# Kernel tuning notes

Hardware: AMD Instinct MI355X
Metric: run time of the kernel (lower is better)

The kernel has to match this reference:

```python
import jax, jax.numpy as jnp
import numpy as np

EPS = 1e-5

def setup_inputs() -> dict:
    key = jax.random.key(0)
    ks = jax.random.split(key, 12)
    b, C, Hx = 8, 1024, 28          # x: (b, C, Hx, Hx); y: (b, C//2, 2*Hx, 2*Hx)
    C2 = C // 2
    r = C2 // 7                      # fc bottleneck = 73
    f32 = jnp.float32
    inp = {
        'y': jax.random.normal(ks[0], (b, C2, 2*Hx, 2*Hx), f32),
        'x': jax.random.normal(ks[1], (b, C, Hx, Hx), f32),
        'fc1_w': jax.random.normal(ks[2], (r, C2), f32) * 0.02,
        'fc2_w': jax.random.normal(ks[3], (C2, r), f32) * 0.02,
        'conv_w': jax.random.normal(ks[4], (C2, C, 1, 1), f32) * 0.02,
        'conv_b': jnp.zeros((C2,), f32),
        'conv1_w': jax.random.normal(ks[5], (C2, C2 * 4, 1, 1), f32) * 0.02,
        'conv1_b': jnp.zeros((C2,), f32),
        'bn_gamma': jnp.ones((C2,), f32),
        'bn_beta': jnp.zeros((C2,), f32),
        'bn_mean': jnp.zeros((C2,), f32),
        'bn_var': jnp.ones((C2,), f32),
        'dw_w': jax.random.normal(ks[6], (C, 1, 3, 3), f32) * 0.1,  # depthwise, groups=C
        'dw_b': jnp.zeros((C,), f32),
    }
    return inp

def reference(y, x, fc1_w, fc2_w, conv_w, conv_b, conv1_w, conv1_b,
              bn_gamma, bn_beta, bn_mean, bn_var, dw_w, dw_b):
    def bn(t):  # BatchNorm2d in eval mode (running stats); same bn module reused twice
        return (t - bn_mean[:, None, None]) * jax.lax.rsqrt(bn_var[:, None, None] + EPS) \
               * bn_gamma[:, None, None] + bn_beta[:, None, None]
    # SE channel attention on y
    s = jnp.mean(y, axis=(2, 3))                              # (b, C2) GAP
    s = jax.nn.relu(s @ fc1_w.T) @ fc2_w.T                    # bias-free FCs
    y1 = y * jax.nn.sigmoid(s)[:, :, None, None]
    # depthwise 3x3 conv on x
    x1 = jax.lax.conv_general_dilated(
        x, dw_w, (1, 1), ((1, 1), (1, 1)),
        feature_group_count=x.shape[1],
        dimension_numbers=('NCHW', 'OIHW', 'NCHW')) + dw_b[None, :, None, None]
    # np.cov per (b, c) map: rows are variables, ddof=1 -> (Xc @ Xc^T)/(W-1)
    Wn = x1.shape[-1]
    xc = x1 - jnp.mean(x1, axis=-1, keepdims=True)
    x2 = jnp.einsum('bchw,bcgw->bchg', xc, xc) / (Wn - 1)     # (b, C, H, H)
    # 1x1 conv C->C2, bn, sigmoid
    x2 = jnp.einsum('bchw,oc->bohw', x2, conv_w[:, :, 0, 0]) + conv_b[None, :, None, None]
    x2 = jax.nn.sigmoid(bn(x2))
    # bilinear upsample x2 (half-pixel == torch align_corners=False)
    def up2(t):
        bb, cc, hh, ww = t.shape
        return jax.image.resize(t, (bb, cc, 2 * hh, 2 * ww), method='bilinear')
    x_up = up2(x)
    x2_up = up2(x2)
    cat = jnp.concatenate([y1, x2_up, x_up], axis=1)          # (b, 4*C2, 2H, 2W)
    out = jnp.einsum('bchw,oc->bohw', cat, conv1_w[:, :, 0, 0]) + conv1_b[None, :, None, None]
    return jax.nn.relu(bn(out))
```

## Files before the change

kernel.cpp:

```cpp
#include <hip/hip_runtime.h>
#include <math.h>

#define EPSV 1e-5f
#define B 8
#define C 1024
#define C2 512
#define RK 73
#define HW 784
#define QW 3136

typedef __attribute__((ext_vector_type(8))) short bf16x8;
typedef __attribute__((ext_vector_type(4))) float f32x4;

__device__ __forceinline__ unsigned short f2bf(float f) {
    unsigned u = __float_as_uint(f);
    return (unsigned short)((u + 0x7fffu + ((u >> 16) & 1u)) >> 16);
}
__device__ __forceinline__ float ld_f(const float* p) { return *p; }
__device__ __forceinline__ float ld_f(const unsigned short* p) {
    return __uint_as_float(((unsigned)*p) << 16);
}

__global__ void gap_kernel(const float* __restrict__ y, float* __restrict__ s0) {
    int bc = blockIdx.x;
    const float* p = y + (size_t)bc * QW;
    float sum = 0.f;
    for (int i = threadIdx.x; i < QW; i += 256) sum += p[i];
    for (int off = 32; off > 0; off >>= 1) sum += __shfl_down(sum, off, 64);
    __shared__ float red[4];
    if ((threadIdx.x & 63) == 0) red[threadIdx.x >> 6] = sum;
    __syncthreads();
    if (threadIdx.x == 0)
        s0[bc] = (red[0] + red[1] + red[2] + red[3]) * (1.0f / QW);
}

__global__ void se_fc_kernel(const float* __restrict__ s0,
                             const float* __restrict__ fc1_w,
                             const float* __restrict__ fc2_w,
                             float* __restrict__ att) {
    int b = blockIdx.x;
    __shared__ float sv[C2];
    __shared__ float hv[RK];
    for (int i = threadIdx.x; i < C2; i += 256) sv[i] = s0[b * C2 + i];
    __syncthreads();
    if (threadIdx.x < RK) {
        float acc = 0.f;
        const float* wr = fc1_w + threadIdx.x * C2;
        for (int k = 0; k < C2; ++k) acc += wr[k] * sv[k];
        hv[threadIdx.x] = fmaxf(acc, 0.f);
    }
    __syncthreads();
    for (int o = threadIdx.x; o < C2; o += 256) {
        float acc = 0.f;
        const float* wr = fc2_w + o * RK;
        for (int j = 0; j < RK; ++j) acc += wr[j] * hv[j];
        att[b * C2 + o] = 1.f / (1.f + expf(-acc));
    }
}

__global__ void dwcov_kernel(const float* __restrict__ x,
                             const float* __restrict__ dw_w,
                             const float* __restrict__ dw_b,
                             unsigned short* __restrict__ cov) {
    int bc = blockIdx.x;
    int c = bc & (C - 1);
    __shared__ float xs[HW];
    __shared__ float x1[HW];
    __shared__ float rm[28];
    const float* px = x + (size_t)bc * HW;
    for (int i = threadIdx.x; i < HW; i += 256) xs[i] = px[i];
    float wk[9];
#pragma unroll
    for (int j = 0; j < 9; ++j) wk[j] = dw_w[c * 9 + j];
    float bias = dw_b[c];
    __syncthreads();
    for (int p = threadIdx.x; p < HW; p += 256) {
        int h = p / 28, w = p - h * 28;
        float acc = bias;
#pragma unroll
        for (int dh = 0; dh < 3; ++dh) {
            int hh = h + dh - 1;
            if (hh < 0 || hh >= 28) continue;
#pragma unroll
            for (int dw = 0; dw < 3; ++dw) {
                int ww = w + dw - 1;
                if (ww < 0 || ww >= 28) continue;
                acc += xs[hh * 28 + ww] * wk[dh * 3 + dw];
            }
        }
        x1[p] = acc;
    }
    __syncthreads();
    if (threadIdx.x < 28) {
        float s = 0.f;
        for (int w = 0; w < 28; ++w) s += x1[threadIdx.x * 28 + w];
        rm[threadIdx.x] = s * (1.f / 28.f);
    }
    __syncthreads();
    unsigned short* pc = cov + (size_t)bc * HW;
    for (int p = threadIdx.x; p < HW; p += 256) {
        int h = p / 28, g = p - h * 28;
        float mh = rm[h], mg = rm[g];
        float acc = 0.f;
        for (int w = 0; w < 28; ++w)
            acc += (x1[h * 28 + w] - mh) * (x1[g * 28 + w] - mg);
        pc[p] = f2bf(acc * (1.f / 27.f));
    }
}

__global__ void pack_w(const float* __restrict__ conv_w, const float* __restrict__ conv_b,
                       const float* __restrict__ conv1_w, const float* __restrict__ conv1_b,
                       const float* __restrict__ bn_g, const float* __restrict__ bn_b,
                       const float* __restrict__ bn_m, const float* __restrict__ bn_v,
                       unsigned short* __restrict__ w0b, unsigned short* __restrict__ w1p0,
                       unsigned short* __restrict__ w1pT,
                       float* __restrict__ sA, float* __restrict__ sB0, float* __restrict__ sB1) {
    int o = blockIdx.x, t = threadIdx.x;
    for (int i = t; i < C; i += 256) w0b[(size_t)o * C + i] = f2bf(conv_w[(size_t)o * C + i]);
    for (int i = t; i < C2; i += 256) w1p0[(size_t)o * C2 + i] = f2bf(conv1_w[(size_t)o * 2048 + i]);
    for (int i = t; i < 1536; i += 256) w1pT[(size_t)o * 1536 + i] = f2bf(conv1_w[(size_t)o * 2048 + 512 + i]);
    if (t == 0) {
        float sc = rsqrtf(bn_v[o] + EPSV) * bn_g[o];
        float bi = bn_b[o] - bn_m[o] * sc;
        sA[o] = sc;
        sB0[o] = conv_b[o] * sc + bi;
        sB1[o] = conv1_b[o] * sc + bi;
    }
}

template<typename ST, bool ATT>
__global__ __launch_bounds__(256)
void transpose_pass(const ST* __restrict__ src, unsigned short* __restrict__ dst,
                    const float* __restrict__ att,
                    int rows, int cols, int dpitch, int doff) {
    int b = blockIdx.z;
    int c0 = blockIdx.y * 64, p0 = blockIdx.x * 64;
    __shared__ float ts[64][65];
    int tid = threadIdx.x;
    int pl = tid & 63, r0 = tid >> 6;
    const ST* sb = src + ((size_t)b * rows + c0) * cols + p0;
    if (p0 + pl < cols) {
#pragma unroll
        for (int j = 0; j < 16; ++j) {
            int cl = r0 + j * 4;
            ts[cl][pl] = ld_f(&sb[(size_t)cl * cols + pl]);
        }
    }
    __syncthreads();
    int cl = tid & 63;
    float av = ATT ? att[b * rows + c0 + cl] : 1.f;
#pragma unroll
    for (int j = 0; j < 16; ++j) {
        int pl2 = r0 + j * 4;
        if (p0 + pl2 < cols)
            dst[((size_t)b * cols + p0 + pl2) * dpitch + doff + c0 + cl] = f2bf(ts[cl][pl2] * av);
    }
}

template<int MODE, int K>
__global__ __launch_bounds__(256)
void mfma_gemm(const unsigned short* __restrict__ wpk,
               const unsigned short* __restrict__ bsrc,
               const unsigned short* __restrict__ Pb,
               const float* __restrict__ sA, const float* __restrict__ sB,
               void* __restrict__ outv) {
    constexpr int NIT = K / 32;
    constexpr int NT  = (MODE == 2) ? 49 : 98;
    constexpr int QN = NT >> 3, REM = NT & 7;
    int bx = blockIdx.x;
    int r = bx & 7, ii = bx >> 3;
    int og = ii & 7, s = ii >> 3;
    int cnt = QN + (r < REM ? 1 : 0);
    if (s >= cnt) return;
    int t = (r < REM ? r * (QN + 1) : REM * (QN + 1) + (r - REM) * QN) + s;
    int o0 = og * 64;
    int n0 = t * 64;
    int b = blockIdx.z;
    union SM {
        struct { __align__(16) unsigned short Wt[2][2560]; __align__(16) unsigned short At[2][2560]; } s;
        float pt[(MODE == 2) ? 64 * 84 : 4];
    };
    __shared__ SM sm;
    int tid = threadIdx.x;
    int lane = tid & 63, wv = tid >> 6;
    int ln = lane & 15, quad = lane >> 4;
    int o_w = (wv >> 1) * 32, q_w = (wv & 1) * 32;
    int swr = tid >> 2, swk = (tid & 3) * 8;
    const unsigned short* wg = wpk + (size_t)(o0 + swr) * K + swk;
    const unsigned short* bg = bsrc + ((size_t)((MODE == 2) ? b * QW : 0) + n0 + swr) * K + swk;

    uint4 stA_a, stA_b, stB_a, stB_b;

#define LD_STAGE(P, CH) {                                                   \
        P##_a = *(const uint4*)(wg + (size_t)(CH) * 32);                    \
        P##_b = *(const uint4*)(bg + (size_t)(CH) * 32); }

#define ST_STAGE(P, BUF) {                                                  \
        *(uint4*)&sm.s.Wt[BUF][swr * 40 + swk] = P##_a;                     \
        *(uint4*)&sm.s.At[BUF][swr * 40 + swk] = P##_b; }

#define GEMM_BODY(BUF, P, CHW, CHL) {                                               \
        bf16x8 af0 = *(const bf16x8*)&sm.s.Wt[BUF][(o_w + ln) * 40 + quad * 8];     \
        bf16x8 af1 = *(const bf16x8*)&sm.s.Wt[BUF][(o_w + 16 + ln) * 40 + quad * 8];\
        bf16x8 bf0 = *(const bf16x8*)&sm.s.At[BUF][(q_w + ln) * 40 + quad * 8];     \
        bf16x8 bf1 = *(const bf16x8*)&sm.s.At[BUF][(q_w + 16 + ln) * 40 + quad * 8];\
        acc[0][0] = __builtin_amdgcn_mfma_f32_16x16x32_bf16(af0, bf0, acc[0][0], 0, 0, 0); \
        acc[0][1] = __builtin_amdgcn_mfma_f32_16x16x32_bf16(af0, bf1, acc[0][1], 0, 0, 0); \
        acc[1][0] = __builtin_amdgcn_mfma_f32_16x16x32_bf16(af1, bf0, acc[1][0], 0, 0, 0); \
        acc[1][1] = __builtin_amdgcn_mfma_f32_16x16x32_bf16(af1, bf1, acc[1][1], 0, 0, 0); \
        if ((CHW) < NIT) {                                                          \
            ST_STAGE(P, (BUF) ^ 1)                                                  \
            if ((CHL) < NIT) LD_STAGE(P, (CHL))                                     \
            asm volatile("s_waitcnt lgkmcnt(0)" ::: "memory");                      \
            __builtin_amdgcn_s_barrier();                                           \
            __builtin_amdgcn_sched_barrier(0);                                      \
        } }

    LD_STAGE(stA, 0)
    ST_STAGE(stA, 0)
    LD_STAGE(stA, 1)
    LD_STAGE(stB, 2)
    asm volatile("s_waitcnt lgkmcnt(0)" ::: "memory");
    __builtin_amdgcn_s_barrier();
    __builtin_amdgcn_sched_barrier(0);

    f32x4 acc[2][2] = {};
    for (int i2 = 0; i2 < NIT; i2 += 2) {
        GEMM_BODY(0, stA, i2 + 1, i2 + 3)
        GEMM_BODY(1, stB, i2 + 2, i2 + 4)
    }
#undef GEMM_BODY
#undef ST_STAGE
#undef LD_STAGE

    if (MODE == 2) {
        float* outp = (float*)outv;
        __syncthreads();
        int h0 = n0 / 56;
        int hmin = (h0 & 1) ? (h0 >> 1) : max(0, (h0 >> 1) - 1);
        for (int e = tid; e < 64 * 84; e += 256) {
            int o_l = e / 84, rem = e - o_l * 84;
            int s2 = rem / 28, w = rem - s2 * 28;
            int row = min(hmin + s2, 27);
            sm.pt[e] = ld_f(&Pb[((size_t)b * C2 + o0 + o_l) * HW + row * 28 + w]);
        }
        __syncthreads();
#pragma unroll
        for (int nt = 0; nt < 2; ++nt) {
            int q = n0 + q_w + nt * 16 + ln;
            int hq = q / 56, wq = q - hq * 56;
            int hm = hq >> 1, wm = wq >> 1;
            int hn = (hq & 1) ? min(hm + 1, 27) : max(hm - 1, 0);
            int wn_ = (wq & 1) ? min(wm + 1, 27) : max(wm - 1, 0);
            int rm_ = (hm - hmin) * 28, rn_ = (hn - hmin) * 28;
#pragma unroll
            for (int mt = 0; mt < 2; ++mt)
#pragma unroll
                for (int reg = 0; reg < 4; ++reg) {
                    int ol = o_w + mt * 16 + quad * 4 + reg;
                    int o = o0 + ol;
                    const float* Pt = &sm.pt[ol * 84];
                    float up = 0.5625f * Pt[rm_ + wm] + 0.1875f * (Pt[rm_ + wn_] + Pt[rn_ + wm])
                             + 0.0625f * Pt[rn_ + wn_];
                    float v = (acc[mt][nt][reg] + up) * sA[o] + sB[o];
                    outp[((size_t)b * C2 + o) * QW + q] = fmaxf(v, 0.f);
                }
        }
    } else if (MODE == 0) {
        unsigned short* outp = (unsigned short*)outv;
#pragma unroll
        for (int nt = 0; nt < 2; ++nt) {
            int n = n0 + q_w + nt * 16 + ln;
#pragma unroll
            for (int mt = 0; mt < 2; ++mt) {
                int ob = o0 + o_w + mt * 16 + quad * 4;
                unsigned short pk[4];
#pragma unroll
                for (int reg = 0; reg < 4; ++reg) {
                    int o = ob + reg;
                    float v = acc[mt][nt][reg] * sA[o] + sB[o];
                    pk[reg] = f2bf(1.f / (1.f + expf(-v)));
                }
                *(uint2*)&outp[(size_t)n * 1536 + ob] = *(uint2*)pk;
            }
        }
    } else {
        unsigned short* outp = (unsigned short*)outv;
#pragma unroll
        for (int nt = 0; nt < 2; ++nt) {
            int n = n0 + q_w + nt * 16 + ln;
            int be = n / HW, pe = n - be * HW;
#pragma unroll
            for (int mt = 0; mt < 2; ++mt)
#pragma unroll
                for (int reg = 0; reg < 4; ++reg) {
                    int o = o0 + o_w + mt * 16 + quad * 4 + reg;
                    outp[((size_t)be * C2 + o) * HW + pe] = f2bf(acc[mt][nt][reg]);
                }
        }
    }
}

extern "C" void kernel_launch(void* const* d_in, const int* in_sizes, int n_in,
                              void* d_out, int out_size, void* d_ws, size_t ws_size,
                              hipStream_t stream) {
    const float* y       = (const float*)d_in[0];
    const float* x       = (const float*)d_in[1];
    const float* fc1_w   = (const float*)d_in[2];
    const float* fc2_w   = (const float*)d_in[3];
    const float* conv_w  = (const float*)d_in[4];
    const float* conv_b  = (const float*)d_in[5];
    const float* conv1_w = (const float*)d_in[6];
    const float* conv1_b = (const float*)d_in[7];
    const float* bn_g    = (const float*)d_in[8];
    const float* bn_b    = (const float*)d_in[9];
    const float* bn_m    = (const float*)d_in[10];
    const float* bn_v    = (const float*)d_in[11];
    const float* dw_w    = (const float*)d_in[12];
    const float* dw_b    = (const float*)d_in[13];
    float* out = (float*)d_out;

    unsigned short* cov_bf = (unsigned short*)d_out;
    unsigned short* covT   = cov_bf + (size_t)B * C * HW;
    unsigned short* BcatT  = covT + (size_t)B * HW * C;

    float* ws  = (float*)d_ws;
    float* s0  = ws;
    float* att = ws + 4096;
    float* sA  = ws + 8192;
    float* sB0 = ws + 8704;
    float* sB1 = ws + 9216;
    unsigned short* w0b  = (unsigned short*)(ws + 9728);
    unsigned short* w1p0 = w0b + (size_t)C2 * C;
    unsigned short* w1pT = w1p0 + (size_t)C2 * C2;
    unsigned short* yT   = w1pT + (size_t)C2 * 1536;
    unsigned short* Pb   = yT + (size_t)B * QW * C2;

    gap_kernel<<<B * C2, 256, 0, stream>>>(y, s0);
    se_fc_kernel<<<B, 256, 0, stream>>>(s0, fc1_w, fc2_w, att);
    pack_w<<<C2, 256, 0, stream>>>(conv_w, conv_b, conv1_w, conv1_b,
                                   bn_g, bn_b, bn_m, bn_v,
                                   w0b, w1p0, w1pT, sA, sB0, sB1);
    dwcov_kernel<<<B * C, 256, 0, stream>>>(x, dw_w, dw_b, cov_bf);
    transpose_pass<float, false><<<dim3(13, 16, B), 256, 0, stream>>>(
        x, BcatT, nullptr, C, HW, 1536, 512);
    transpose_pass<unsigned short, false><<<dim3(13, 16, B), 256, 0, stream>>>(
        cov_bf, covT, nullptr, C, HW, C, 0);
    transpose_pass<float, true><<<dim3(49, 8, B), 256, 0, stream>>>(
        y, yT, att, C2, QW, C2, 0);
    mfma_gemm<0, 1024><<<dim3(832), 256, 0, stream>>>(w0b, covT, nullptr, sA, sB0, BcatT);
    mfma_gemm<1, 1536><<<dim3(832), 256, 0, stream>>>(w1pT, BcatT, nullptr, sA, sB0, Pb);
    mfma_gemm<2, 512><<<dim3(448, 1, B), 256, 0, stream>>>(w1p0, yT, Pb, sA, sB1, out);
}
```

Before: 328.0 us.

## Enlarge MFMA GEMM tiles to 128x128 with XOR-swizzled LDS layout

Raises the GEMM block tile from 64x64 to 128x128 so each wave computes a 64x64 subtile with a 4x4 MFMA accumulator array. LDS rows drop the padding and use an XOR swizzle to avoid bank conflicts. The goal is more data reuse per LDS load and less global traffic per FLOP. The grids shrink to match (224 and 128x8 blocks), which lowers block-level parallelism. The MODE 2 epilogue now stages the upsample patch in two halves and guards the partial last tile. Register pressure rises, and the launch bound of 3 blocks per SM may force spills.

```diff
diff --git a/kernel.cpp b/kernel.cpp
--- a/kernel.cpp
+++ b/kernel.cpp
@@ -158,56 +158,78 @@
 }
 
 template<int MODE, int K>
-__global__ __launch_bounds__(256)
+__global__ __launch_bounds__(256, 3)
 void mfma_gemm(const unsigned short* __restrict__ wpk,
                const unsigned short* __restrict__ bsrc,
                const unsigned short* __restrict__ Pb,
                const float* __restrict__ sA, const float* __restrict__ sB,
                void* __restrict__ outv) {
     constexpr int NIT = K / 32;
-    constexpr int NT  = (MODE == 2) ? 49 : 98;
+    constexpr int NT  = (MODE == 2) ? 25 : 49;
     constexpr int QN = NT >> 3, REM = NT & 7;
     int bx = blockIdx.x;
     int r = bx & 7, ii = bx >> 3;
-    int og = ii & 7, s = ii >> 3;
+    int og = ii & 3, s = ii >> 2;
     int cnt = QN + (r < REM ? 1 : 0);
     if (s >= cnt) return;
     int t = (r < REM ? r * (QN + 1) : REM * (QN + 1) + (r - REM) * QN) + s;
-    int o0 = og * 64;
-    int n0 = t * 64;
+    int o0 = og * 128;
+    int n0 = t * 128;
     int b = blockIdx.z;
     union SM {
-        struct { __align__(16) unsigned short Wt[2][2560]; __align__(16) unsigned short At[2][2560]; } s;
-        float pt[(MODE == 2) ? 64 * 84 : 4];
+        struct { __align__(16) unsigned short Wt[2][4096]; __align__(16) unsigned short At[2][4096]; } s;
+        float pt[(MODE == 2) ? 64 * 140 : 4];
     };
     __shared__ SM sm;
     int tid = threadIdx.x;
     int lane = tid & 63, wv = tid >> 6;
     int ln = lane & 15, quad = lane >> 4;
-    int o_w = (wv >> 1) * 32, q_w = (wv & 1) * 32;
-    int swr = tid >> 2, swk = (tid & 3) * 8;
-    const unsigned short* wg = wpk + (size_t)(o0 + swr) * K + swk;
-    const unsigned short* bg = bsrc + ((size_t)((MODE == 2) ? b * QW : 0) + n0 + swr) * K + swk;
-
-    uint4 stA_a, stA_b, stB_a, stB_b;
+    int wr = wv >> 1, wc = wv & 1;
+    int srow = tid >> 2, schk = tid & 3;
+    int stw = srow * 32 + ((schk ^ ((srow >> 1) & 3)) << 3);
+    int rq  = (quad ^ ((ln >> 1) & 3)) << 3;
+    const unsigned short* wg0 = wpk + (size_t)(o0 + srow) * K + schk * 8;
+    const unsigned short* wg1 = wg0 + (size_t)64 * K;
+    const unsigned short* bg0;
+    const unsigned short* bg1;
+    if (MODE == 2) {
+        int q0 = min(n0 + srow, QW - 1);
+        int q1 = min(n0 + srow + 64, QW - 1);
+        bg0 = bsrc + ((size_t)b * QW + q0) * K + schk * 8;
+        bg1 = bsrc + ((size_t)b * QW + q1) * K + schk * 8;
+    } else {
+        bg0 = bsrc + (size_t)(n0 + srow) * K + schk * 8;
+        bg1 = bg0 + (size_t)64 * K;
+    }
+
+    uint4 stA_a0, stA_a1, stA_b0, stA_b1;
+    uint4 stB_a0, stB_a1, stB_b0, stB_b1;
 
 #define LD_STAGE(P, CH) {                                                   \
-        P##_a = *(const uint4*)(wg + (size_t)(CH) * 32);                    \
-        P##_b = *(const uint4*)(bg + (size_t)(CH) * 32); }
+        P##_a0 = *(const uint4*)(wg0 + (size_t)(CH) * 32);                  \
+        P##_a1 = *(const uint4*)(wg1 + (size_t)(CH) * 32);                  \
+        P##_b0 = *(const uint4*)(bg0 + (size_t)(CH) * 32);                  \
+        P##_b1 = *(const uint4*)(bg1 + (size_t)(CH) * 32); }
 
 #define ST_STAGE(P, BUF) {                                                  \
-        *(uint4*)&sm.s.Wt[BUF][swr * 40 + swk] = P##_a;                     \
-        *(uint4*)&sm.s.At[BUF][swr * 40 + swk] = P##_b; }
+        *(uint4*)&sm.s.Wt[BUF][stw] = P##_a0;                               \
+        *(uint4*)&sm.s.Wt[BUF][stw + 2048] = P##_a1;                        \
+        *(uint4*)&sm.s.At[BUF][stw] = P##_b0;                               \
+        *(uint4*)&sm.s.At[BUF][stw + 2048] = P##_b1; }
 
 #define GEMM_BODY(BUF, P, CHW, CHL) {                                               \
-        bf16x8 af0 = *(const bf16x8*)&sm.s.Wt[BUF][(o_w + ln) * 40 + quad * 8];     \
-        bf16x8 af1 = *(const bf16x8*)&sm.s.Wt[BUF][(o_w + 16 + ln) * 40 + quad * 8];\
-        bf16x8 bf0 = *(const bf16x8*)&sm.s.At[BUF][(q_w + ln) * 40 + quad * 8];     \
-        bf16x8 bf1 = *(const bf16x8*)&sm.s.At[BUF][(q_w + 16 + ln) * 40 + quad * 8];\
-        acc[0][0] = __builtin_amdgcn_mfma_f32_16x16x32_bf16(af0, bf0, acc[0][0], 0, 0, 0); \
-        acc[0][1] = __builtin_amdgcn_mfma_f32_16x16x32_bf16(af0, bf1, acc[0][1], 0, 0, 0); \
-        acc[1][0] = __builtin_amdgcn_mfma_f32_16x16x32_bf16(af1, bf0, acc[1][0], 0, 0, 0); \
-        acc[1][1] = __builtin_amdgcn_mfma_f32_16x16x32_bf16(af1, bf1, acc[1][1], 0, 0, 0); \
+        bf16x8 af[4], bf[4];                                                        \
+        _Pragma("unroll")                                                           \
+        for (int mt = 0; mt < 4; ++mt)                                              \
+            af[mt] = *(const bf16x8*)&sm.s.Wt[BUF][wr * 2048 + (mt * 16 + ln) * 32 + rq]; \
+        _Pragma("unroll")                                                           \
+        for (int nt = 0; nt < 4; ++nt)                                              \
+            bf[nt] = *(const bf16x8*)&sm.s.At[BUF][wc * 2048 + (nt * 16 + ln) * 32 + rq]; \
+        _Pragma("unroll")                                                           \
+        for (int mt = 0; mt < 4; ++mt)                                              \
+            _Pragma("unroll")                                                       \
+            for (int nt = 0; nt < 4; ++nt)                                          \
+                acc[mt][nt] = __builtin_amdgcn_mfma_f32_16x16x32_bf16(af[mt], bf[nt], acc[mt][nt], 0, 0, 0); \
         if ((CHW) < NIT) {                                                          \
             ST_STAGE(P, (BUF) ^ 1)                                                  \
             if ((CHL) < NIT) LD_STAGE(P, (CHL))                                     \
@@ -224,7 +246,7 @@
     __builtin_amdgcn_s_barrier();
     __builtin_amdgcn_sched_barrier(0);
 
-    f32x4 acc[2][2] = {};
+    f32x4 acc[4][4] = {};
     for (int i2 = 0; i2 < NIT; i2 += 2) {
         GEMM_BODY(0, stA, i2 + 1, i2 + 3)
         GEMM_BODY(1, stB, i2 + 2, i2 + 4)
@@ -235,45 +257,52 @@
 
     if (MODE == 2) {
         float* outp = (float*)outv;
-        __syncthreads();
         int h0 = n0 / 56;
-        int hmin = (h0 & 1) ? (h0 >> 1) : max(0, (h0 >> 1) - 1);
-        for (int e = tid; e < 64 * 84; e += 256) {
-            int o_l = e / 84, rem = e - o_l * 84;
-            int s2 = rem / 28, w = rem - s2 * 28;
-            int row = min(hmin + s2, 27);
-            sm.pt[e] = ld_f(&Pb[((size_t)b * C2 + o0 + o_l) * HW + row * 28 + w]);
-        }
-        __syncthreads();
-#pragma unroll
-        for (int nt = 0; nt < 2; ++nt) {
-            int q = n0 + q_w + nt * 16 + ln;
-            int hq = q / 56, wq = q - hq * 56;
-            int hm = hq >> 1, wm = wq >> 1;
-            int hn = (hq & 1) ? min(hm + 1, 27) : max(hm - 1, 0);
-            int wn_ = (wq & 1) ? min(wm + 1, 27) : max(wm - 1, 0);
-            int rm_ = (hm - hmin) * 28, rn_ = (hn - hmin) * 28;
-#pragma unroll
-            for (int mt = 0; mt < 2; ++mt)
-#pragma unroll
-                for (int reg = 0; reg < 4; ++reg) {
-                    int ol = o_w + mt * 16 + quad * 4 + reg;
-                    int o = o0 + ol;
-                    const float* Pt = &sm.pt[ol * 84];
-                    float up = 0.5625f * Pt[rm_ + wm] + 0.1875f * (Pt[rm_ + wn_] + Pt[rn_ + wm])
-                             + 0.0625f * Pt[rn_ + wn_];
-                    float v = (acc[mt][nt][reg] + up) * sA[o] + sB[o];
-                    outp[((size_t)b * C2 + o) * QW + q] = fmaxf(v, 0.f);
+        int hmin = max(0, (h0 >> 1) - 1);
+#pragma unroll
+        for (int hi = 0; hi < 2; ++hi) {
+            __syncthreads();
+            for (int e = tid; e < 64 * 140; e += 256) {
+                int o_l = e / 140, rem = e - o_l * 140;
+                int s2 = rem / 28, w = rem - s2 * 28;
+                int row = min(hmin + s2, 27);
+                sm.pt[e] = ld_f(&Pb[((size_t)b * C2 + o0 + hi * 64 + o_l) * HW + row * 28 + w]);
+            }
+            __syncthreads();
+            if (wr == hi) {
+#pragma unroll
+                for (int nt = 0; nt < 4; ++nt) {
+                    int q = n0 + wc * 64 + nt * 16 + ln;
+                    if (q < QW) {
+                        int hq = q / 56, wq = q - hq * 56;
+                        int hm = hq >> 1, wm = wq >> 1;
+                        int hn = (hq & 1) ? min(hm + 1, 27) : max(hm - 1, 0);
+                        int wn_ = (wq & 1) ? min(wm + 1, 27) : max(wm - 1, 0);
+                        int rm_ = (hm - hmin) * 28, rn_ = (hn - hmin) * 28;
+#pragma unroll
+                        for (int mt = 0; mt < 4; ++mt)
+#pragma unroll
+                            for (int reg = 0; reg < 4; ++reg) {
+                                int ol = mt * 16 + quad * 4 + reg;
+                                int o = o0 + hi * 64 + ol;
+                                const float* Pt = &sm.pt[ol * 140];
+                                float up = 0.5625f * Pt[rm_ + wm] + 0.1875f * (Pt[rm_ + wn_] + Pt[rn_ + wm])
+                                         + 0.0625f * Pt[rn_ + wn_];
+                                float v = (acc[mt][nt][reg] + up) * sA[o] + sB[o];
+                                outp[((size_t)b * C2 + o) * QW + q] = fmaxf(v, 0.f);
+                            }
+                    }
                 }
+            }
         }
     } else if (MODE == 0) {
         unsigned short* outp = (unsigned short*)outv;
 #pragma unroll
-        for (int nt = 0; nt < 2; ++nt) {
-            int n = n0 + q_w + nt * 16 + ln;
-#pragma unroll
-            for (int mt = 0; mt < 2; ++mt) {
-                int ob = o0 + o_w + mt * 16 + quad * 4;
+        for (int nt = 0; nt < 4; ++nt) {
+            int n = n0 + wc * 64 + nt * 16 + ln;
+#pragma unroll
+            for (int mt = 0; mt < 4; ++mt) {
+                int ob = o0 + wr * 64 + mt * 16 + quad * 4;
                 unsigned short pk[4];
 #pragma unroll
                 for (int reg = 0; reg < 4; ++reg) {
@@ -287,14 +316,14 @@
     } else {
         unsigned short* outp = (unsigned short*)outv;
 #pragma unroll
-        for (int nt = 0; nt < 2; ++nt) {
-            int n = n0 + q_w + nt * 16 + ln;
+        for (int nt = 0; nt < 4; ++nt) {
+            int n = n0 + wc * 64 + nt * 16 + ln;
             int be = n / HW, pe = n - be * HW;
 #pragma unroll
-            for (int mt = 0; mt < 2; ++mt)
+            for (int mt = 0; mt < 4; ++mt)
 #pragma unroll
                 for (int reg = 0; reg < 4; ++reg) {
-                    int o = o0 + o_w + mt * 16 + quad * 4 + reg;
+                    int o = o0 + wr * 64 + mt * 16 + quad * 4 + reg;
                     outp[((size_t)be * C2 + o) * HW + pe] = f2bf(acc[mt][nt][reg]);
                 }
         }
@@ -348,7 +377,7 @@
         cov_bf, covT, nullptr, C, HW, C, 0);
     transpose_pass<float, true><<<dim3(49, 8, B), 256, 0, stream>>>(
         y, yT, att, C2, QW, C2, 0);
-    mfma_gemm<0, 1024><<<dim3(832), 256, 0, stream>>>(w0b, covT, nullptr, sA, sB0, BcatT);
-    mfma_gemm<1, 1536><<<dim3(832), 256, 0, stream>>>(w1pT, BcatT, nullptr, sA, sB0, Pb);
-    mfma_gemm<2, 512><<<dim3(448, 1, B), 256, 0, stream>>>(w1p0, yT, Pb, sA, sB1, out);
-}
+    mfma_gemm<0, 1024><<<dim3(224), 256, 0, stream>>>(w0b, covT, nullptr, sA, sB0, BcatT);
+    mfma_gemm<1, 1536><<<dim3(224), 256, 0, stream>>>(w1pT, BcatT, nullptr, sA, sB0, Pb);
+    mfma_gemm<2, 512><<<dim3(128, 1, B), 256, 0, stream>>>(w1p0, yT, Pb, sA, sB1, out);
+}
```

New measurement: 352.0 us. +7.3%, slower.

## Fuse GAP into y transpose and fold SE attention into per-batch weights

Applied to the files above, without the earlier changes.

Removes the separate global-average-pool pass over y: the y transpose now accumulates channel sums through atomicAdd while it transposes, after a small zero-init kernel. The SE sigmoid scale is no longer applied to y during the transpose. It is folded into a per-batch copy of the conv1 weight slice built in pack_w, and the final GEMM indexes weights by batch. This saves one full read of y (about 51 MB) at the cost of 8x more weight packing, float atomics, and a changed rounding order for the attention scale. It also vectorizes the fc1 dot product and prefetches the Pb tile into registers before the barrier in the final GEMM epilogue.

```diff
diff --git a/kernel.cpp b/kernel.cpp
--- a/kernel.cpp
+++ b/kernel.cpp
@@ -21,17 +21,8 @@
     return __uint_as_float(((unsigned)*p) << 16);
 }
 
-__global__ void gap_kernel(const float* __restrict__ y, float* __restrict__ s0) {
-    int bc = blockIdx.x;
-    const float* p = y + (size_t)bc * QW;
-    float sum = 0.f;
-    for (int i = threadIdx.x; i < QW; i += 256) sum += p[i];
-    for (int off = 32; off > 0; off >>= 1) sum += __shfl_down(sum, off, 64);
-    __shared__ float red[4];
-    if ((threadIdx.x & 63) == 0) red[threadIdx.x >> 6] = sum;
-    __syncthreads();
-    if (threadIdx.x == 0)
-        s0[bc] = (red[0] + red[1] + red[2] + red[3]) * (1.0f / QW);
+__global__ void zero_s0(float* __restrict__ s0) {
+    s0[blockIdx.x * 256 + threadIdx.x] = 0.f;
 }
 
 __global__ void se_fc_kernel(const float* __restrict__ s0,
@@ -41,18 +32,24 @@
     int b = blockIdx.x;
     __shared__ float sv[C2];
     __shared__ float hv[RK];
-    for (int i = threadIdx.x; i < C2; i += 256) sv[i] = s0[b * C2 + i];
+    for (int i = threadIdx.x; i < C2; i += 256) sv[i] = s0[b * C2 + i] * (1.0f / QW);
     __syncthreads();
     if (threadIdx.x < RK) {
         float acc = 0.f;
-        const float* wr = fc1_w + threadIdx.x * C2;
-        for (int k = 0; k < C2; ++k) acc += wr[k] * sv[k];
+        const float4* wr4 = (const float4*)(fc1_w + threadIdx.x * C2);
+        const float4* sv4 = (const float4*)sv;
+#pragma unroll 16
+        for (int k = 0; k < C2 / 4; ++k) {
+            float4 w4 = wr4[k], s4 = sv4[k];
+            acc += w4.x * s4.x + w4.y * s4.y + w4.z * s4.z + w4.w * s4.w;
+        }
         hv[threadIdx.x] = fmaxf(acc, 0.f);
     }
     __syncthreads();
     for (int o = threadIdx.x; o < C2; o += 256) {
         float acc = 0.f;
         const float* wr = fc2_w + o * RK;
+#pragma unroll
         for (int j = 0; j < RK; ++j) acc += wr[j] * hv[j];
         att[b * C2 + o] = 1.f / (1.f + expf(-acc));
     }
@@ -112,13 +109,17 @@
                        const float* __restrict__ conv1_w, const float* __restrict__ conv1_b,
                        const float* __restrict__ bn_g, const float* __restrict__ bn_b,
                        const float* __restrict__ bn_m, const float* __restrict__ bn_v,
-                       unsigned short* __restrict__ w0b, unsigned short* __restrict__ w1p0,
+                       const float* __restrict__ att,
+                       unsigned short* __restrict__ w0b, unsigned short* __restrict__ w1y,
                        unsigned short* __restrict__ w1pT,
                        float* __restrict__ sA, float* __restrict__ sB0, float* __restrict__ sB1) {
     int o = blockIdx.x, t = threadIdx.x;
     for (int i = t; i < C; i += 256) w0b[(size_t)o * C + i] = f2bf(conv_w[(size_t)o * C + i]);
-    for (int i = t; i < C2; i += 256) w1p0[(size_t)o * C2 + i] = f2bf(conv1_w[(size_t)o * 2048 + i]);
     for (int i = t; i < 1536; i += 256) w1pT[(size_t)o * 1536 + i] = f2bf(conv1_w[(size_t)o * 2048 + 512 + i]);
+#pragma unroll
+    for (int b = 0; b < B; ++b)
+        for (int c2 = t; c2 < C2; c2 += 256)
+            w1y[((size_t)b * C2 + o) * C2 + c2] = f2bf(conv1_w[(size_t)o * 2048 + c2] * att[b * C2 + c2]);
     if (t == 0) {
         float sc = rsqrtf(bn_v[o] + EPSV) * bn_g[o];
         float bi = bn_b[o] - bn_m[o] * sc;
@@ -128,10 +129,10 @@
     }
 }
 
-template<typename ST, bool ATT>
+template<typename ST, bool GAP>
 __global__ __launch_bounds__(256)
 void transpose_pass(const ST* __restrict__ src, unsigned short* __restrict__ dst,
-                    const float* __restrict__ att,
+                    float* __restrict__ s0,
                     int rows, int cols, int dpitch, int doff) {
     int b = blockIdx.z;
     int c0 = blockIdx.y * 64, p0 = blockIdx.x * 64;
@@ -148,12 +149,19 @@
     }
     __syncthreads();
     int cl = tid & 63;
-    float av = ATT ? att[b * rows + c0 + cl] : 1.f;
 #pragma unroll
     for (int j = 0; j < 16; ++j) {
         int pl2 = r0 + j * 4;
         if (p0 + pl2 < cols)
-            dst[((size_t)b * cols + p0 + pl2) * dpitch + doff + c0 + cl] = f2bf(ts[cl][pl2] * av);
+            dst[((size_t)b * cols + p0 + pl2) * dpitch + doff + c0 + cl] = f2bf(ts[cl][pl2]);
+    }
+    if (GAP) {
+        if (tid < 64) {
+            float s = 0.f;
+#pragma unroll
+            for (int i = 0; i < 64; ++i) s += ts[tid][i];
+            atomicAdd(&s0[b * rows + c0 + tid], s);
+        }
     }
 }
 
@@ -186,7 +194,8 @@
     int ln = lane & 15, quad = lane >> 4;
     int o_w = (wv >> 1) * 32, q_w = (wv & 1) * 32;
     int swr = tid >> 2, swk = (tid & 3) * 8;
-    const unsigned short* wg = wpk + (size_t)(o0 + swr) * K + swk;
+    const unsigned short* wp = (MODE == 2) ? wpk + (size_t)b * C2 * C2 : wpk;
+    const unsigned short* wg = wp + (size_t)(o0 + swr) * K + swk;
     const unsigned short* bg = bsrc + ((size_t)((MODE == 2) ? b * QW : 0) + n0 + swr) * K + swk;
 
     uint4 stA_a, stA_b, stB_a, stB_b;
@@ -235,15 +244,20 @@
 
     if (MODE == 2) {
         float* outp = (float*)outv;
-        __syncthreads();
         int h0 = n0 / 56;
         int hmin = (h0 & 1) ? (h0 >> 1) : max(0, (h0 >> 1) - 1);
-        for (int e = tid; e < 64 * 84; e += 256) {
+        float stv[21];
+#pragma unroll
+        for (int j = 0; j < 21; ++j) {
+            int e = tid + j * 256;
             int o_l = e / 84, rem = e - o_l * 84;
             int s2 = rem / 28, w = rem - s2 * 28;
             int row = min(hmin + s2, 27);
-            sm.pt[e] = ld_f(&Pb[((size_t)b * C2 + o0 + o_l) * HW + row * 28 + w]);
-        }
+            stv[j] = ld_f(&Pb[((size_t)b * C2 + o0 + o_l) * HW + row * 28 + w]);
+        }
+        __syncthreads();
+#pragma unroll
+        for (int j = 0; j < 21; ++j) sm.pt[tid + j * 256] = stv[j];
         __syncthreads();
 #pragma unroll
         for (int nt = 0; nt < 2; ++nt) {
@@ -331,24 +345,24 @@
     float* sB0 = ws + 8704;
     float* sB1 = ws + 9216;
     unsigned short* w0b  = (unsigned short*)(ws + 9728);
-    unsigned short* w1p0 = w0b + (size_t)C2 * C;
-    unsigned short* w1pT = w1p0 + (size_t)C2 * C2;
+    unsigned short* w1y  = w0b + (size_t)C2 * C;
+    unsigned short* w1pT = w1y + (size_t)B * C2 * C2;
     unsigned short* yT   = w1pT + (size_t)C2 * 1536;
     unsigned short* Pb   = yT + (size_t)B * QW * C2;
 
-    gap_kernel<<<B * C2, 256, 0, stream>>>(y, s0);
+    zero_s0<<<16, 256, 0, stream>>>(s0);
+    transpose_pass<float, true><<<dim3(49, 8, B), 256, 0, stream>>>(
+        y, yT, s0, C2, QW, C2, 0);
     se_fc_kernel<<<B, 256, 0, stream>>>(s0, fc1_w, fc2_w, att);
     pack_w<<<C2, 256, 0, stream>>>(conv_w, conv_b, conv1_w, conv1_b,
-                                   bn_g, bn_b, bn_m, bn_v,
-                                   w0b, w1p0, w1pT, sA, sB0, sB1);
+                                   bn_g, bn_b, bn_m, bn_v, att,
+                                   w0b, w1y, w1pT, sA, sB0, sB1);
     dwcov_kernel<<<B * C, 256, 0, stream>>>(x, dw_w, dw_b, cov_bf);
     transpose_pass<float, false><<<dim3(13, 16, B), 256, 0, stream>>>(
         x, BcatT, nullptr, C, HW, 1536, 512);
     transpose_pass<unsigned short, false><<<dim3(13, 16, B), 256, 0, stream>>>(
         cov_bf, covT, nullptr, C, HW, C, 0);
-    transpose_pass<float, true><<<dim3(49, 8, B), 256, 0, stream>>>(
-        y, yT, att, C2, QW, C2, 0);
     mfma_gemm<0, 1024><<<dim3(832), 256, 0, stream>>>(w0b, covT, nullptr, sA, sB0, BcatT);
     mfma_gemm<1, 1536><<<dim3(832), 256, 0, stream>>>(w1pT, BcatT, nullptr, sA, sB0, Pb);
-    mfma_gemm<2, 512><<<dim3(448, 1, B), 256, 0, stream>>>(w1p0, yT, Pb, sA, sB1, out);
-}
+    mfma_gemm<2, 512><<<dim3(448, 1, B), 256, 0, stream>>>(w1y, yT, Pb, sA, sB1, out);
+}
```

Result: faster. 313.3 us (-4.5%).
